# Performance work log

Measured on AMD Instinct MI355X. Metric: run time of the kernel, lower is better.

## Reference

```python
import jax, jax.numpy as jnp
import numpy as np
import math

B, S, H = 2, 2048, 1024
NH, HD = 16, 64  # num heads, head dim; NH*HD == H


def setup_inputs() -> dict:
    key = jax.random.key(0)
    k1, k2, k3 = jax.random.split(key, 3)
    hidden_states = jax.random.normal(k1, (B, S, H), dtype=jnp.float32)
    # causal multiplicative mask [1,1,S,S], 1.0 where attending is allowed
    mask = jnp.tril(jnp.ones((S, S), dtype=jnp.float32))[None, None]
    W_qkv = jax.random.normal(k2, (H, 3 * H), dtype=jnp.float32) * (1.0 / math.sqrt(H))
    b_qkv = jnp.zeros((3 * H,), dtype=jnp.float32)
    W_out = jax.random.normal(k3, (H, H), dtype=jnp.float32) * (1.0 / math.sqrt(H))
    b_out = jnp.zeros((H,), dtype=jnp.float32)
    return {"hidden_states": hidden_states, "mask": mask, "W_qkv": W_qkv,
            "b_qkv": b_qkv, "W_out": W_out, "b_out": b_out}


def reference(hidden_states, mask, W_qkv, b_qkv, W_out, b_out):
    b, s, h = hidden_states.shape
    # fused QKV projection then split into contiguous thirds (split_tensor_along_last_dim)
    qkv = jnp.einsum('bsh,hd->bsd', hidden_states, W_qkv) + b_qkv
    q, k, v = jnp.split(qkv, 3, axis=-1)
    # [b, s, nh*hd] -> [b, nh, s, hd]
    def to_heads(t):
        return t.reshape(b, s, NH, HD).transpose(0, 2, 1, 3)
    q, k, v = to_heads(q), to_heads(k), to_heads(v)
    q = q / jnp.sqrt(jnp.float32(HD))  # scaling_attention_score=True
    scores = jnp.einsum('bhqd,bhkd->bhqk', q, k)  # [b,nh,s,s]
    # multiplicative mask + large-negative bias trick from standard_attention
    scores = scores * mask - 10000.0 * (1.0 - mask)
    probs = jax.nn.softmax(scores, axis=-1)
    ctx = jnp.einsum('bhqk,bhkd->bhqd', probs, v)
    ctx = ctx.transpose(0, 2, 1, 3).reshape(b, s, h)  # [b, s, nh*hd]
    return jnp.einsum('bsh,hd->bsd', ctx, W_out) + b_out
```

## Files before the change

### kernel.cpp

```cpp
#include <hip/hip_runtime.h>
#include <cstdint>
#include <cstddef>

#define NHEAD 16
#define HDIM 64
#define SEQ 2048
#define BATCH 2
#define HID 1024

typedef __bf16 bf16x8 __attribute__((ext_vector_type(8)));
typedef float f32x4 __attribute__((ext_vector_type(4)));

__device__ __forceinline__ unsigned short f2bf(float f) {
    union { float f; unsigned u; } v; v.f = f;
    unsigned r = v.u + 0x7fffu + ((v.u >> 16) & 1u);
    return (unsigned short)(r >> 16);
}

__device__ __forceinline__ unsigned cvtpk_bf16(float a, float b) {
    unsigned d;
    asm("v_cvt_pk_bf16_f32 %0, %1, %2" : "=v"(d) : "v"(a), "v"(b));
    return d;
}

__global__ __launch_bounds__(256) void convert_f32_bf16(
    const float* __restrict__ in, unsigned short* __restrict__ out, int n) {
    int i = (blockIdx.x * 256 + threadIdx.x) * 8;
    if (i >= n) return;
    float4 a = *(const float4*)(in + i);
    float4 b = *(const float4*)(in + i + 4);
    uint4 o;
    o.x = (unsigned)f2bf(a.x) | ((unsigned)f2bf(a.y) << 16);
    o.y = (unsigned)f2bf(a.z) | ((unsigned)f2bf(a.w) << 16);
    o.z = (unsigned)f2bf(b.x) | ((unsigned)f2bf(b.y) << 16);
    o.w = (unsigned)f2bf(b.z) | ((unsigned)f2bf(b.w) << 16);
    *(uint4*)(out + i) = o;
}

__global__ __launch_bounds__(256) void transpose_f32_bf16(
    const float* __restrict__ in, unsigned short* __restrict__ out, int R, int C) {
    __shared__ unsigned short T[64][72];
    int t = threadIdx.x;
    int c0 = blockIdx.x * 64, r0 = blockIdx.y * 64;
    for (int p = 0; p < 4; ++p) {
        int idx = (p * 256 + t) * 4;
        int row = idx >> 6, col = idx & 63;
        float4 v = *(const float4*)(in + (size_t)(r0 + row) * C + c0 + col);
        T[row][col + 0] = f2bf(v.x);
        T[row][col + 1] = f2bf(v.y);
        T[row][col + 2] = f2bf(v.z);
        T[row][col + 3] = f2bf(v.w);
    }
    __syncthreads();
    for (int p = 0; p < 4; ++p) {
        int idx = (p * 256 + t) * 4;
        int orow = idx >> 6, ocol = idx & 63;
        ushort4 u;
        u.x = T[ocol + 0][orow];
        u.y = T[ocol + 1][orow];
        u.z = T[ocol + 2][orow];
        u.w = T[ocol + 3][orow];
        *(ushort4*)(out + (size_t)(c0 + orow) * R + r0 + ocol) = u;
    }
}

#define GEMM_BODY(Aptr, Btptr, KDIM, BX, BY)                                             \
    __shared__ unsigned short As[128][32];                                               \
    __shared__ unsigned short Bs[128][32];                                               \
    int t = threadIdx.x;                                                                 \
    int wave = t >> 6, lane = t & 63, ln = lane & 15, quad = lane >> 4;                  \
    int wm = wave >> 1, wn = wave & 1;                                                   \
    int m0 = (BY) * 128, n0 = (BX) * 128;                                                \
    int srow = lane >> 2, scol = (lane & 3) * 8;                                         \
    f32x4 zero4 = {0.f, 0.f, 0.f, 0.f};                                                  \
    f32x4 acc[4][4];                                                                     \
    for (int mi = 0; mi < 4; ++mi)                                                       \
        for (int ni = 0; ni < 4; ++ni) acc[mi][ni] = zero4;                              \
    for (int kt = 0; kt < (KDIM); kt += 32) {                                            \
        for (int p = 0; p < 2; ++p) {                                                    \
            int r0 = (wave * 2 + p) * 16 + srow;                                         \
            __builtin_amdgcn_global_load_lds(                                            \
                (const __attribute__((address_space(1))) void*)                          \
                    ((Aptr) + (size_t)(m0 + r0) * (KDIM) + kt + scol),                   \
                (__attribute__((address_space(3))) void*)&As[(wave * 2 + p) * 16][0],    \
                16, 0, 0);                                                               \
            __builtin_amdgcn_global_load_lds(                                            \
                (const __attribute__((address_space(1))) void*)                          \
                    ((Btptr) + (size_t)(n0 + r0) * (KDIM) + kt + scol),                  \
                (__attribute__((address_space(3))) void*)&Bs[(wave * 2 + p) * 16][0],    \
                16, 0, 0);                                                               \
        }                                                                                \
        __syncthreads();                                                                 \
        bf16x8 af[4], bfr[4];                                                            \
        for (int mi = 0; mi < 4; ++mi)                                                   \
            af[mi] = *(const bf16x8*)&As[wm * 64 + mi * 16 + ln][quad * 8];              \
        for (int ni = 0; ni < 4; ++ni)                                                   \
            bfr[ni] = *(const bf16x8*)&Bs[wn * 64 + ni * 16 + ln][quad * 8];             \
        for (int mi = 0; mi < 4; ++mi)                                                   \
            for (int ni = 0; ni < 4; ++ni)                                               \
                acc[mi][ni] = __builtin_amdgcn_mfma_f32_16x16x32_bf16(                   \
                    af[mi], bfr[ni], acc[mi][ni], 0, 0, 0);                              \
        __syncthreads();                                                                 \
    }

__global__ __launch_bounds__(256) void gemm_qkv(
    const unsigned short* __restrict__ A, const unsigned short* __restrict__ Bt,
    const float* __restrict__ bias,
    unsigned short* __restrict__ Qb, unsigned short* __restrict__ Kb,
    unsigned short* __restrict__ Vt) {
    int fid = blockIdx.y * 24 + blockIdx.x;
    int xcd = fid & 7, jj = fid >> 3;
    int by = (xcd & 3) * 8 + jj / 12;
    int bx = (xcd >> 2) * 12 + jj % 12;
    GEMM_BODY(A, Bt, 1024, bx, by)
    int nbase = n0 + wn * 64;
    for (int ni = 0; ni < 4; ++ni) {
        int gn = nbase + ni * 16 + ln;
        float bv = bias[gn];
        int third = gn >> 10;
        int rem = gn & 1023;
        int h = rem >> 6, d = rem & 63;
        if (third == 2) {
            for (int mi = 0; mi < 4; ++mi) {
                int gm = m0 + wm * 64 + mi * 16 + quad * 4;
                int b = gm >> 11, s = gm & 2047;
                size_t bh = (size_t)(b * NHEAD + h);
                ushort4 u;
                u.x = f2bf(acc[mi][ni][0] + bv);
                u.y = f2bf(acc[mi][ni][1] + bv);
                u.z = f2bf(acc[mi][ni][2] + bv);
                u.w = f2bf(acc[mi][ni][3] + bv);
                *(ushort4*)&Vt[(bh * HDIM + d) * SEQ + s] = u;
            }
        } else {
            unsigned short* dst = third == 0 ? Qb : Kb;
            float scale = third == 0 ? 0.1803368801111f : 1.0f;
            for (int mi = 0; mi < 4; ++mi) {
                for (int r = 0; r < 4; ++r) {
                    int gm = m0 + wm * 64 + mi * 16 + quad * 4 + r;
                    int b = gm >> 11, s = gm & 2047;
                    size_t bh = (size_t)(b * NHEAD + h);
                    dst[(bh * SEQ + s) * HDIM + d] = f2bf((acc[mi][ni][r] + bv) * scale);
                }
            }
        }
    }
}

__global__ __launch_bounds__(256) void gemm_out(
    const unsigned short* __restrict__ A, const unsigned short* __restrict__ Bt,
    const float* __restrict__ bias, float* __restrict__ C) {
    int fid = blockIdx.y * 8 + blockIdx.x;
    int xcd = fid & 7, jj = fid >> 3;
    int by = xcd * 4 + (jj >> 3);
    int bx = jj & 7;
    GEMM_BODY(A, Bt, 1024, bx, by)
    int nbase = n0 + wn * 64;
    for (int ni = 0; ni < 4; ++ni) {
        int gn = nbase + ni * 16 + ln;
        float bv = bias[gn];
        for (int mi = 0; mi < 4; ++mi) {
            for (int r = 0; r < 4; ++r) {
                int gm = m0 + wm * 64 + mi * 16 + quad * 4 + r;
                C[(size_t)gm * HID + gn] = acc[mi][ni][r] + bv;
            }
        }
    }
}

__global__ __launch_bounds__(256, 2) void flash_attn(
    const unsigned short* __restrict__ Qb, const unsigned short* __restrict__ Kb,
    const unsigned short* __restrict__ Vt, unsigned short* __restrict__ Ctx) {
    __shared__ unsigned short KsB[2][64][64];
    __shared__ unsigned short VsB[2][64][64];
    __shared__ unsigned short Ps[2][4][16][72];
    int tid = threadIdx.x;
    int wave = tid >> 6, lane = tid & 63, ln = lane & 15, quad = lane >> 4;

    int id = blockIdx.y * 16 + blockIdx.x;
    int xcd = id & 7, j = id >> 3;
    int bh = xcd * 4 + (j & 3);
    int r0 = (j >> 2) & 7;
    int bxrole = (j < 32) ? r0 : 15 - r0;
    int qiA = bxrole;
    int qiB = 31 - bxrole;
    int q0A = qiA * 64, q0B = qiB * 64;
    const size_t baseQK = (size_t)bh * SEQ * HDIM;
    const size_t baseV = (size_t)bh * HDIM * SEQ;
    int b = bh >> 4, h = bh & 15;

    int rIn = lane >> 3;
    int gsw = ((lane & 7) ^ rIn) * 8;

    bf16x8 aqA0, aqA1, aqB0, aqB1;
    {
        const unsigned short* qp =
            Qb + baseQK + (size_t)(q0A + wave * 16 + ln) * HDIM + quad * 8;
        aqA0 = *(const bf16x8*)qp;
        aqA1 = *(const bf16x8*)(qp + 32);
        qp = Qb + baseQK + (size_t)(q0B + wave * 16 + ln) * HDIM + quad * 8;
        aqB0 = *(const bf16x8*)qp;
        aqB1 = *(const bf16x8*)(qp + 32);
    }

    auto prefetch = [&](int kj, int bi) {
        const unsigned short* kb = Kb + baseQK + (size_t)kj * 64 * HDIM;
        const unsigned short* vb = Vt + baseV + kj * 64;
        for (int c = wave; c < 8; c += 4) {
            __builtin_amdgcn_global_load_lds(
                (const __attribute__((address_space(1))) void*)(kb + (c * 8 + rIn) * HDIM + gsw),
                (__attribute__((address_space(3))) void*)&KsB[bi][c * 8][0], 16, 0, 0);
            __builtin_amdgcn_global_load_lds(
                (const __attribute__((address_space(1))) void*)(vb + (size_t)(c * 8 + rIn) * SEQ + gsw),
                (__attribute__((address_space(3))) void*)&VsB[bi][c * 8][0], 16, 0, 0);
        }
    };

    f32x4 zero4 = {0.f, 0.f, 0.f, 0.f};
    f32x4 oA[4], oB[4];
    float laccA = 0.f, laccB = 0.f;
    for (int i = 0; i < 4; ++i) { oA[i] = zero4; oB[i] = zero4; }

    auto epilogue = [&](const f32x4* o, float lacc, int q0) {
        float sum = lacc;
        sum += __shfl_xor(sum, 16);
        sum += __shfl_xor(sum, 32);
        float linv = __builtin_amdgcn_rcpf(sum);
        size_t rowb = ((size_t)(b * SEQ + q0 + wave * 16 + ln)) * HID + h * 64;
        for (int ni = 0; ni < 4; ++ni) {
            ushort4 u;
            u.x = f2bf(o[ni][0] * linv);
            u.y = f2bf(o[ni][1] * linv);
            u.z = f2bf(o[ni][2] * linv);
            u.w = f2bf(o[ni][3] * linv);
            *(ushort4*)&Ctx[rowb + ni * 16 + quad * 4] = u;
        }
    };

    prefetch(0, 0);
    for (int t = 0; t <= qiB; ++t) {
        __syncthreads();
        if (t < qiB) prefetch(t + 1, (t + 1) & 1);
        int buf = t & 1;
        bool joint = (t <= qiA);

        bf16x8 akf[2][4];
#pragma unroll
        for (int kk = 0; kk < 2; ++kk)
#pragma unroll
            for (int ni = 0; ni < 4; ++ni)
                akf[kk][ni] = *(const bf16x8*)
                    &KsB[buf][ni * 16 + ln][((kk * 4 + quad) ^ (ln & 7)) * 8];
        f32x4 sA[4], sB[4];
#pragma unroll
        for (int ni = 0; ni < 4; ++ni) { sA[ni] = zero4; sB[ni] = zero4; }
        __builtin_amdgcn_s_setprio(1);
#pragma unroll
        for (int kk = 0; kk < 2; ++kk) {
            bf16x8 bq = kk ? aqB1 : aqB0;
#pragma unroll
            for (int ni = 0; ni < 4; ++ni)
                sB[ni] = __builtin_amdgcn_mfma_f32_16x16x32_bf16(akf[kk][ni], bq, sB[ni], 0, 0, 0);
        }
        if (joint) {
#pragma unroll
            for (int kk = 0; kk < 2; ++kk) {
                bf16x8 bq = kk ? aqA1 : aqA0;
#pragma unroll
                for (int ni = 0; ni < 4; ++ni)
                    sA[ni] = __builtin_amdgcn_mfma_f32_16x16x32_bf16(akf[kk][ni], bq, sA[ni], 0, 0, 0);
            }
        }
        __builtin_amdgcn_s_setprio(0);

        if (t == qiB) {
#pragma unroll
            for (int ni = 0; ni < 4; ++ni)
#pragma unroll
                for (int r = 0; r < 4; ++r)
                    if (ni * 16 + quad * 4 + r > wave * 16 + ln) sB[ni][r] = -1.0e38f;
        }
        if (t == qiA) {
#pragma unroll
            for (int ni = 0; ni < 4; ++ni)
#pragma unroll
                for (int r = 0; r < 4; ++r)
                    if (ni * 16 + quad * 4 + r > wave * 16 + ln) sA[ni][r] = -1.0e38f;
        }

#pragma unroll
        for (int ni = 0; ni < 4; ++ni) {
            float e0 = __builtin_amdgcn_exp2f(sB[ni][0]);
            float e1 = __builtin_amdgcn_exp2f(sB[ni][1]);
            float e2 = __builtin_amdgcn_exp2f(sB[ni][2]);
            float e3 = __builtin_amdgcn_exp2f(sB[ni][3]);
            laccB += (e0 + e1) + (e2 + e3);
            uint2 pw;
            pw.x = cvtpk_bf16(e0, e1);
            pw.y = cvtpk_bf16(e2, e3);
            *(uint2*)&Ps[0][wave][ln][ni * 16 + quad * 4] = pw;
        }
        if (joint) {
#pragma unroll
            for (int ni = 0; ni < 4; ++ni) {
                float e0 = __builtin_amdgcn_exp2f(sA[ni][0]);
                float e1 = __builtin_amdgcn_exp2f(sA[ni][1]);
                float e2 = __builtin_amdgcn_exp2f(sA[ni][2]);
                float e3 = __builtin_amdgcn_exp2f(sA[ni][3]);
                laccA += (e0 + e1) + (e2 + e3);
                uint2 pw;
                pw.x = cvtpk_bf16(e0, e1);
                pw.y = cvtpk_bf16(e2, e3);
                *(uint2*)&Ps[1][wave][ln][ni * 16 + quad * 4] = pw;
            }
        }

        bf16x8 avf[2][4];
#pragma unroll
        for (int kk = 0; kk < 2; ++kk)
#pragma unroll
            for (int ni = 0; ni < 4; ++ni)
                avf[kk][ni] = *(const bf16x8*)
                    &VsB[buf][ni * 16 + ln][((kk * 4 + quad) ^ (ln & 7)) * 8];
        {
            bf16x8 bp0 = *(const bf16x8*)&Ps[0][wave][ln][quad * 8];
            bf16x8 bp1 = *(const bf16x8*)&Ps[0][wave][ln][32 + quad * 8];
            __builtin_amdgcn_s_setprio(1);
#pragma unroll
            for (int ni = 0; ni < 4; ++ni)
                oB[ni] = __builtin_amdgcn_mfma_f32_16x16x32_bf16(avf[0][ni], bp0, oB[ni], 0, 0, 0);
#pragma unroll
            for (int ni = 0; ni < 4; ++ni)
                oB[ni] = __builtin_amdgcn_mfma_f32_16x16x32_bf16(avf[1][ni], bp1, oB[ni], 0, 0, 0);
            __builtin_amdgcn_s_setprio(0);
        }
        if (joint) {
            bf16x8 bp0 = *(const bf16x8*)&Ps[1][wave][ln][quad * 8];
            bf16x8 bp1 = *(const bf16x8*)&Ps[1][wave][ln][32 + quad * 8];
            __builtin_amdgcn_s_setprio(1);
#pragma unroll
            for (int ni = 0; ni < 4; ++ni)
                oA[ni] = __builtin_amdgcn_mfma_f32_16x16x32_bf16(avf[0][ni], bp0, oA[ni], 0, 0, 0);
#pragma unroll
            for (int ni = 0; ni < 4; ++ni)
                oA[ni] = __builtin_amdgcn_mfma_f32_16x16x32_bf16(avf[1][ni], bp1, oA[ni], 0, 0, 0);
            __builtin_amdgcn_s_setprio(0);
        }

        if (t == qiA) epilogue(oA, laccA, q0A);
        if (t == qiB) epilogue(oB, laccB, q0B);
    }
}

extern "C" void kernel_launch(void* const* d_in, const int* in_sizes, int n_in,
                              void* d_out, int out_size, void* d_ws, size_t ws_size,
                              hipStream_t stream) {
    const float* X = (const float*)d_in[0];
    const float* Wqkv = (const float*)d_in[2];
    const float* bqkv = (const float*)d_in[3];
    const float* Wout = (const float*)d_in[4];
    const float* bout = (const float*)d_in[5];
    float* out = (float*)d_out;

    char* ws = (char*)d_ws;
    unsigned short* Xb   = (unsigned short*)(ws + 0);
    unsigned short* W1t  = (unsigned short*)(ws + 8388608);
    unsigned short* W2t  = (unsigned short*)(ws + 14680064);
    unsigned short* Qb   = (unsigned short*)(ws + 16777216);
    unsigned short* Kb   = (unsigned short*)(ws + 25165824);
    unsigned short* Vt   = (unsigned short*)(ws + 33554432);
    unsigned short* Ctx  = (unsigned short*)(ws + 41943040);

    convert_f32_bf16<<<2048, 256, 0, stream>>>(X, Xb, 4194304);
    transpose_f32_bf16<<<dim3(48, 16), 256, 0, stream>>>(Wqkv, W1t, 1024, 3072);
    transpose_f32_bf16<<<dim3(16, 16), 256, 0, stream>>>(Wout, W2t, 1024, 1024);
    gemm_qkv<<<dim3(24, 32), 256, 0, stream>>>(Xb, W1t, bqkv, Qb, Kb, Vt);
    flash_attn<<<dim3(16, 32), 256, 0, stream>>>(Qb, Kb, Vt, Ctx);
    gemm_out<<<dim3(8, 32), 256, 0, stream>>>(Ctx, W2t, bout, out);
}
```

Measured before the change: 206.0 us.

## Rewrite QKV GEMM with 256x256 tiles and multi-stage LDS pipeline

Replaces the QKV projection GEMM with a 512-thread, 256x256-tile kernel. It uses a six-slot A / four-slot B ring buffer in LDS with XOR-swizzled global_load_lds staging, fine-grained vmcnt waits and barriers, and s_setprio around the MFMA bursts. The aim is to overlap global loads with MFMA work and raise data reuse per tile, removing the load-then-compute stalls of the old single-buffered 128x128 kernel. The trade-offs are fewer blocks (192) for the GPU, which may leave CUs idle, and much more complex synchronisation. gemm_out is left unchanged, now written inline instead of through the macro.

```diff
diff --git a/kernel.cpp b/kernel.cpp
--- a/kernel.cpp
+++ b/kernel.cpp
@@ -10,6 +10,9 @@
 
 typedef __bf16 bf16x8 __attribute__((ext_vector_type(8)));
 typedef float f32x4 __attribute__((ext_vector_type(4)));
+
+#define AS1 __attribute__((address_space(1)))
+#define AS3 __attribute__((address_space(3)))
 
 __device__ __forceinline__ unsigned short f2bf(float f) {
     union { float f; unsigned u; } v; v.f = f;
@@ -64,83 +67,135 @@
     }
 }
 
-#define GEMM_BODY(Aptr, Btptr, KDIM, BX, BY)                                             \
-    __shared__ unsigned short As[128][32];                                               \
-    __shared__ unsigned short Bs[128][32];                                               \
-    int t = threadIdx.x;                                                                 \
-    int wave = t >> 6, lane = t & 63, ln = lane & 15, quad = lane >> 4;                  \
-    int wm = wave >> 1, wn = wave & 1;                                                   \
-    int m0 = (BY) * 128, n0 = (BX) * 128;                                                \
-    int srow = lane >> 2, scol = (lane & 3) * 8;                                         \
-    f32x4 zero4 = {0.f, 0.f, 0.f, 0.f};                                                  \
-    f32x4 acc[4][4];                                                                     \
-    for (int mi = 0; mi < 4; ++mi)                                                       \
-        for (int ni = 0; ni < 4; ++ni) acc[mi][ni] = zero4;                              \
-    for (int kt = 0; kt < (KDIM); kt += 32) {                                            \
-        for (int p = 0; p < 2; ++p) {                                                    \
-            int r0 = (wave * 2 + p) * 16 + srow;                                         \
-            __builtin_amdgcn_global_load_lds(                                            \
-                (const __attribute__((address_space(1))) void*)                          \
-                    ((Aptr) + (size_t)(m0 + r0) * (KDIM) + kt + scol),                   \
-                (__attribute__((address_space(3))) void*)&As[(wave * 2 + p) * 16][0],    \
-                16, 0, 0);                                                               \
-            __builtin_amdgcn_global_load_lds(                                            \
-                (const __attribute__((address_space(1))) void*)                          \
-                    ((Btptr) + (size_t)(n0 + r0) * (KDIM) + kt + scol),                  \
-                (__attribute__((address_space(3))) void*)&Bs[(wave * 2 + p) * 16][0],    \
-                16, 0, 0);                                                               \
-        }                                                                                \
-        __syncthreads();                                                                 \
-        bf16x8 af[4], bfr[4];                                                            \
-        for (int mi = 0; mi < 4; ++mi)                                                   \
-            af[mi] = *(const bf16x8*)&As[wm * 64 + mi * 16 + ln][quad * 8];              \
-        for (int ni = 0; ni < 4; ++ni)                                                   \
-            bfr[ni] = *(const bf16x8*)&Bs[wn * 64 + ni * 16 + ln][quad * 8];             \
-        for (int mi = 0; mi < 4; ++mi)                                                   \
-            for (int ni = 0; ni < 4; ++ni)                                               \
-                acc[mi][ni] = __builtin_amdgcn_mfma_f32_16x16x32_bf16(                   \
-                    af[mi], bfr[ni], acc[mi][ni], 0, 0, 0);                              \
-        __syncthreads();                                                                 \
-    }
-
-__global__ __launch_bounds__(256) void gemm_qkv(
+__global__ __launch_bounds__(512, 2) void gemm_qkv(
     const unsigned short* __restrict__ A, const unsigned short* __restrict__ Bt,
     const float* __restrict__ bias,
     unsigned short* __restrict__ Qb, unsigned short* __restrict__ Kb,
     unsigned short* __restrict__ Vt) {
-    int fid = blockIdx.y * 24 + blockIdx.x;
-    int xcd = fid & 7, jj = fid >> 3;
-    int by = (xcd & 3) * 8 + jj / 12;
-    int bx = (xcd >> 2) * 12 + jj % 12;
-    GEMM_BODY(A, Bt, 1024, bx, by)
+    __shared__ unsigned short LDSu[81920];
+    const int NT = 16;
+    int tid = threadIdx.x;
+    int wave = tid >> 6, lane = tid & 63, ln = lane & 15, quad = lane >> 4;
+    int wm = wave >> 2, wn = wave & 3;
+    int fid = blockIdx.y * 12 + blockIdx.x;
+    int xcd = fid & 7, jj0 = fid >> 3;
+    int by = (xcd & 3) * 4 + jj0 / 6;
+    int bx = (xcd >> 2) * 6 + jj0 % 6;
+    int m0 = by * 256, n0 = bx * 256;
+
+    int rsub = lane >> 3;
+    int gs = (lane & 7) ^ rsub;
+
+    auto stage = [&](int h) {
+        if (h >= 4 * NT) return;
+        int T = h >> 2, jj = h & 3;
+        const unsigned short* src;
+        int slot;
+        if (jj < 2) {
+            slot = (2 * T + jj) % 6;
+            src = A + (size_t)(m0 + jj * 128) * 1024 + T * 64;
+        } else {
+            slot = 6 + (2 * T + (jj - 2)) % 4;
+            src = Bt + (size_t)(n0 + (jj - 2) * 128) * 1024 + T * 64;
+        }
+#pragma unroll
+        for (int p = 0; p < 2; ++p) {
+            __builtin_amdgcn_global_load_lds(
+                (const AS1 void*)(src + (size_t)(p * 64 + wave * 8 + rsub) * 1024 + gs * 8),
+                (AS3 void*)&LDSu[slot * 8192 + (p * 8 + wave) * 512], 16, 0, 0);
+        }
+    };
+
+    f32x4 zero4 = {0.f, 0.f, 0.f, 0.f};
+    f32x4 acc[8][4];
+#pragma unroll
+    for (int i = 0; i < 8; ++i)
+#pragma unroll
+        for (int k = 0; k < 4; ++k) acc[i][k] = zero4;
+
+    for (int h = 0; h < 6; ++h) stage(h);
+    asm volatile("s_waitcnt vmcnt(4)" ::: "memory");
+    __builtin_amdgcn_s_barrier();
+
+    for (int t = 0; t < NT; ++t) {
+        int myA = (2 * t + wm) % 6;
+        int myB = 6 + (2 * t + (wn >> 1)) % 4;
+        const unsigned short* as = &LDSu[myA * 8192];
+        const unsigned short* bs = &LDSu[myB * 8192];
+        int brow = (wn & 1) * 64;
+        bf16x8 bfr[4][2];
+#pragma unroll
+        for (int j = 0; j < 4; ++j) {
+            if (j == 0) {
+#pragma unroll
+                for (int fn = 0; fn < 4; ++fn)
+#pragma unroll
+                    for (int ks = 0; ks < 2; ++ks)
+                        bfr[fn][ks] = *(const bf16x8*)
+                            &bs[(brow + fn * 16 + ln) * 64 + (((ks * 4 + quad) ^ (ln & 7)) * 8)];
+            }
+            bf16x8 af[2][2];
+#pragma unroll
+            for (int mi = 0; mi < 2; ++mi)
+#pragma unroll
+                for (int ks = 0; ks < 2; ++ks)
+                    af[mi][ks] = *(const bf16x8*)
+                        &as[((2 * j + mi) * 16 + ln) * 64 + (((ks * 4 + quad) ^ (ln & 7)) * 8)];
+            stage(4 * t + j + 6);
+            if (j == 3 && t < NT - 1) {
+                if (t == NT - 2) asm volatile("s_waitcnt vmcnt(0)" ::: "memory");
+                else             asm volatile("s_waitcnt vmcnt(4)" ::: "memory");
+            }
+            __builtin_amdgcn_s_barrier();
+            asm volatile("s_waitcnt lgkmcnt(0)" ::: "memory");
+            __builtin_amdgcn_sched_barrier(0);
+            __builtin_amdgcn_s_setprio(1);
+#pragma unroll
+            for (int mi = 0; mi < 2; ++mi)
+#pragma unroll
+                for (int fn = 0; fn < 4; ++fn) {
+                    acc[2 * j + mi][fn] = __builtin_amdgcn_mfma_f32_16x16x32_bf16(
+                        af[mi][0], bfr[fn][0], acc[2 * j + mi][fn], 0, 0, 0);
+                    acc[2 * j + mi][fn] = __builtin_amdgcn_mfma_f32_16x16x32_bf16(
+                        af[mi][1], bfr[fn][1], acc[2 * j + mi][fn], 0, 0, 0);
+                }
+            __builtin_amdgcn_s_setprio(0);
+            __builtin_amdgcn_s_barrier();
+        }
+    }
+
     int nbase = n0 + wn * 64;
-    for (int ni = 0; ni < 4; ++ni) {
-        int gn = nbase + ni * 16 + ln;
+#pragma unroll
+    for (int fn = 0; fn < 4; ++fn) {
+        int gn = nbase + fn * 16 + ln;
         float bv = bias[gn];
         int third = gn >> 10;
         int rem = gn & 1023;
         int h = rem >> 6, d = rem & 63;
         if (third == 2) {
-            for (int mi = 0; mi < 4; ++mi) {
-                int gm = m0 + wm * 64 + mi * 16 + quad * 4;
+#pragma unroll
+            for (int fm = 0; fm < 8; ++fm) {
+                int gm = m0 + wm * 128 + fm * 16 + quad * 4;
                 int b = gm >> 11, s = gm & 2047;
                 size_t bh = (size_t)(b * NHEAD + h);
                 ushort4 u;
-                u.x = f2bf(acc[mi][ni][0] + bv);
-                u.y = f2bf(acc[mi][ni][1] + bv);
-                u.z = f2bf(acc[mi][ni][2] + bv);
-                u.w = f2bf(acc[mi][ni][3] + bv);
+                u.x = f2bf(acc[fm][fn][0] + bv);
+                u.y = f2bf(acc[fm][fn][1] + bv);
+                u.z = f2bf(acc[fm][fn][2] + bv);
+                u.w = f2bf(acc[fm][fn][3] + bv);
                 *(ushort4*)&Vt[(bh * HDIM + d) * SEQ + s] = u;
             }
         } else {
             unsigned short* dst = third == 0 ? Qb : Kb;
             float scale = third == 0 ? 0.1803368801111f : 1.0f;
-            for (int mi = 0; mi < 4; ++mi) {
+#pragma unroll
+            for (int fm = 0; fm < 8; ++fm) {
+#pragma unroll
                 for (int r = 0; r < 4; ++r) {
-                    int gm = m0 + wm * 64 + mi * 16 + quad * 4 + r;
+                    int gm = m0 + wm * 128 + fm * 16 + quad * 4 + r;
                     int b = gm >> 11, s = gm & 2047;
                     size_t bh = (size_t)(b * NHEAD + h);
-                    dst[(bh * SEQ + s) * HDIM + d] = f2bf((acc[mi][ni][r] + bv) * scale);
+                    dst[(bh * SEQ + s) * HDIM + d] = f2bf((acc[fm][fn][r] + bv) * scale);
                 }
             }
         }
@@ -150,11 +205,43 @@
 __global__ __launch_bounds__(256) void gemm_out(
     const unsigned short* __restrict__ A, const unsigned short* __restrict__ Bt,
     const float* __restrict__ bias, float* __restrict__ C) {
+    __shared__ unsigned short As[128][32];
+    __shared__ unsigned short Bs[128][32];
+    int t = threadIdx.x;
+    int wave = t >> 6, lane = t & 63, ln = lane & 15, quad = lane >> 4;
+    int wm = wave >> 1, wn = wave & 1;
     int fid = blockIdx.y * 8 + blockIdx.x;
     int xcd = fid & 7, jj = fid >> 3;
     int by = xcd * 4 + (jj >> 3);
     int bx = jj & 7;
-    GEMM_BODY(A, Bt, 1024, bx, by)
+    int m0 = by * 128, n0 = bx * 128;
+    int srow = lane >> 2, scol = (lane & 3) * 8;
+    f32x4 zero4 = {0.f, 0.f, 0.f, 0.f};
+    f32x4 acc[4][4];
+    for (int mi = 0; mi < 4; ++mi)
+        for (int ni = 0; ni < 4; ++ni) acc[mi][ni] = zero4;
+    for (int kt = 0; kt < 1024; kt += 32) {
+        for (int p = 0; p < 2; ++p) {
+            int r0 = (wave * 2 + p) * 16 + srow;
+            __builtin_amdgcn_global_load_lds(
+                (const AS1 void*)(A + (size_t)(m0 + r0) * 1024 + kt + scol),
+                (AS3 void*)&As[(wave * 2 + p) * 16][0], 16, 0, 0);
+            __builtin_amdgcn_global_load_lds(
+                (const AS1 void*)(Bt + (size_t)(n0 + r0) * 1024 + kt + scol),
+                (AS3 void*)&Bs[(wave * 2 + p) * 16][0], 16, 0, 0);
+        }
+        __syncthreads();
+        bf16x8 af[4], bfr[4];
+        for (int mi = 0; mi < 4; ++mi)
+            af[mi] = *(const bf16x8*)&As[wm * 64 + mi * 16 + ln][quad * 8];
+        for (int ni = 0; ni < 4; ++ni)
+            bfr[ni] = *(const bf16x8*)&Bs[wn * 64 + ni * 16 + ln][quad * 8];
+        for (int mi = 0; mi < 4; ++mi)
+            for (int ni = 0; ni < 4; ++ni)
+                acc[mi][ni] = __builtin_amdgcn_mfma_f32_16x16x32_bf16(
+                    af[mi], bfr[ni], acc[mi][ni], 0, 0, 0);
+        __syncthreads();
+    }
     int nbase = n0 + wn * 64;
     for (int ni = 0; ni < 4; ++ni) {
         int gn = nbase + ni * 16 + ln;
@@ -208,11 +295,11 @@
         const unsigned short* vb = Vt + baseV + kj * 64;
         for (int c = wave; c < 8; c += 4) {
             __builtin_amdgcn_global_load_lds(
-                (const __attribute__((address_space(1))) void*)(kb + (c * 8 + rIn) * HDIM + gsw),
-                (__attribute__((address_space(3))) void*)&KsB[bi][c * 8][0], 16, 0, 0);
+                (const AS1 void*)(kb + (c * 8 + rIn) * HDIM + gsw),
+                (AS3 void*)&KsB[bi][c * 8][0], 16, 0, 0);
             __builtin_amdgcn_global_load_lds(
-                (const __attribute__((address_space(1))) void*)(vb + (size_t)(c * 8 + rIn) * SEQ + gsw),
-                (__attribute__((address_space(3))) void*)&VsB[bi][c * 8][0], 16, 0, 0);
+                (const AS1 void*)(vb + (size_t)(c * 8 + rIn) * SEQ + gsw),
+                (AS3 void*)&VsB[bi][c * 8][0], 16, 0, 0);
         }
     };
 
@@ -374,7 +461,7 @@
     convert_f32_bf16<<<2048, 256, 0, stream>>>(X, Xb, 4194304);
     transpose_f32_bf16<<<dim3(48, 16), 256, 0, stream>>>(Wqkv, W1t, 1024, 3072);
     transpose_f32_bf16<<<dim3(16, 16), 256, 0, stream>>>(Wout, W2t, 1024, 1024);
-    gemm_qkv<<<dim3(24, 32), 256, 0, stream>>>(Xb, W1t, bqkv, Qb, Kb, Vt);
+    gemm_qkv<<<dim3(12, 16), 512, 0, stream>>>(Xb, W1t, bqkv, Qb, Kb, Vt);
     flash_attn<<<dim3(16, 32), 256, 0, stream>>>(Qb, Kb, Vt, Ctx);
     gemm_out<<<dim3(8, 32), 256, 0, stream>>>(Ctx, W2t, bout, out);
 }
```

New measurement: 197.0 us. 1.05x faster.
